# Optimization experiments

Hardware: AMD Instinct MI355X
Metric: run time of the kernel (lower is better)

The kernel has to match this reference:

```python
import jax, jax.numpy as jnp
import numpy as np

EMBED = 128
HEADS = 8
HEAD_DIM = EMBED // HEADS

def setup_inputs() -> dict:
    key = jax.random.key(0)
    ks = jax.random.split(key, 8)
    B, N = 2, 4096
    values = jax.random.normal(ks[0], (B, N, EMBED), dtype=jnp.float32)
    keys = jax.random.normal(ks[1], (B, N, EMBED), dtype=jnp.float32)
    query = jax.random.normal(ks[2], (B, N, EMBED), dtype=jnp.float32)
    s = 1.0 / np.sqrt(HEAD_DIM)
    Wv = jax.random.normal(ks[3], (HEAD_DIM, HEAD_DIM), dtype=jnp.float32) * s
    Wk = jax.random.normal(ks[4], (HEAD_DIM, HEAD_DIM), dtype=jnp.float32) * s
    Wq = jax.random.normal(ks[5], (HEAD_DIM, HEAD_DIM), dtype=jnp.float32) * s
    Wo = jax.random.normal(ks[6], (EMBED, EMBED), dtype=jnp.float32) * (1.0 / np.sqrt(EMBED))
    bo = jnp.zeros((EMBED,), dtype=jnp.float32)
    return {"values": values, "keys": keys, "query": query,
            "Wv": Wv, "Wk": Wk, "Wq": Wq, "Wo": Wo, "bo": bo}

def reference(values, keys, query, Wv, Wk, Wq, Wo, bo):
    B, N, _ = query.shape
    # split heads: [B,N,H,Dh]
    v = values.reshape(B, N, HEADS, HEAD_DIM)
    k = keys.reshape(B, N, HEADS, HEAD_DIM)
    q = query.reshape(B, N, HEADS, HEAD_DIM)
    # per-head linear (torch Linear: x @ W.T), same weight for all heads
    v = jnp.einsum('bnhd,ed->bnhe', v, Wv)
    k = jnp.einsum('bnhd,ed->bnhe', k, Wk)
    q = jnp.einsum('bnhd,ed->bnhe', q, Wq)
    # scores [B,H,N,N], note scale by sqrt(embed_size) as in original
    energy = jnp.einsum('bqhd,bkhd->bhqk', q, k) / jnp.sqrt(jnp.float32(EMBED))
    attn = jax.nn.softmax(energy, axis=-1)
    out = jnp.einsum('bhql,blhd->bqhd', attn, v).reshape(B, N, EMBED)
    return out @ Wo.T + bo
```

## Files before the change

### kernel.cpp

```cpp
#include <hip/hip_runtime.h>

#define BB 2
#define NN 4096
#define HH 8
#define DD 16
#define EE 128
#define LBLK 128
#define NSPL 4
#define NIV 4

typedef _Float16 f16;
typedef _Float16 f16x4 __attribute__((ext_vector_type(4)));
typedef _Float16 f16x2 __attribute__((ext_vector_type(2)));
typedef _Float16 f16x8 __attribute__((ext_vector_type(8)));
typedef __fp16 h16x2 __attribute__((ext_vector_type(2)));
typedef float f32x4 __attribute__((ext_vector_type(4)));

#define QSCALE 0.12751741f

__global__ __launch_bounds__(256) void proj_kernel(
    const float* __restrict__ vals, const float* __restrict__ keys,
    const float* __restrict__ query,
    const float* __restrict__ Wv, const float* __restrict__ Wk,
    const float* __restrict__ Wq, const float* __restrict__ Wo,
    f16* __restrict__ Qp, f16* __restrict__ Kp, f16* __restrict__ Vt,
    f16* __restrict__ Wo16)
{
    if (blockIdx.x >= 768) {
        const int i = (blockIdx.x - 768) * 256 + threadIdx.x;
        Wo16[i] = (f16)Wo[i];
        return;
    }
    __shared__ float W[256];
    const int p = blockIdx.x >> 8;
    const float* Wsrc = (p == 0) ? Wv : ((p == 1) ? Wk : Wq);
    W[threadIdx.x] = Wsrc[threadIdx.x];
    __syncthreads();

    const int idx = ((blockIdx.x & 255) << 8) | threadIdx.x;
    const int n = idx & 4095;
    const int h = (idx >> 12) & 7;
    const int b = idx >> 15;

    const float* xsrc = (p == 0) ? vals : ((p == 1) ? keys : query);
    const float4* xp = (const float4*)(xsrc + (size_t)(b * NN + n) * EE + h * DD);
    const float4 x0 = xp[0], x1 = xp[1], x2 = xp[2], x3 = xp[3];
    const float scale = (p == 2) ? QSCALE : 1.0f;

    alignas(16) f16 out[16];
    #pragma unroll
    for (int e = 0; e < 16; e++) {
        const float4* wr = (const float4*)(W + e * 16);
        const float4 w0 = wr[0], w1 = wr[1], w2 = wr[2], w3 = wr[3];
        float acc = x0.x * w0.x + x0.y * w0.y + x0.z * w0.z + x0.w * w0.w
                  + x1.x * w1.x + x1.y * w1.y + x1.z * w1.z + x1.w * w1.w
                  + x2.x * w2.x + x2.y * w2.y + x2.z * w2.z + x2.w * w2.w
                  + x3.x * w3.x + x3.y * w3.y + x3.z * w3.z + x3.w * w3.w;
        out[e] = (f16)(acc * scale);
    }

    if (p == 0) {
        f16* dst = Vt + (size_t)(b * HH + h) * DD * NN + n;
        #pragma unroll
        for (int e = 0; e < 16; e++) dst[(size_t)e * NN] = out[e];
    } else {
        f16* dst = ((p == 1) ? Kp : Qp) + (size_t)((b * HH + h) * NN + n) * DD;
        ((uint4*)dst)[0] = ((const uint4*)out)[0];
        ((uint4*)dst)[1] = ((const uint4*)out)[1];
    }
}

__global__ __launch_bounds__(512, 8) void attn_kernel(
    const f16* __restrict__ Qp, const f16* __restrict__ Kp,
    const f16* __restrict__ Vt, f16* __restrict__ Oacc,
    float* __restrict__ den)
{
    __shared__ alignas(16) f16 Kl[2][2][2048];
    __shared__ alignas(16) f16 Vl[2][2][2048];

    const int tid = threadIdx.x;
    const int lane = tid & 63;
    const int wave = tid >> 6;
    const int r = lane & 15;
    const int g = lane >> 4;

    const int bid = blockIdx.x;
    const int quarter = bid & 3;
    const int bh = (bid >> 2) & 15;
    const int qt = bid >> 6;
    const int q0 = qt * 256 + wave * 32;
    const int L0 = quarter * (NN / NSPL);

    const int ti = tid >> 8;
    const int u = tid & 255;
    const bool isK = u < 128;
    const f16* gbase;
    int w0, w1;
    if (isK) {
        const int spair = u >> 6;
        const int lp = u & 63;
        const int rr = lp & 15, gg = lp >> 4;
        const int lam = 8 * (rr >> 2) + (rr & 3);
        gbase = Kp + ((size_t)bh * NN + L0 + ti * LBLK + 64 * spair + lam) * DD + 4 * gg;
        w0 = (2 * spair) * 512 + lp * 8;
        w1 = (2 * spair + 1) * 512 + lp * 8;
    } else {
        const int v = u - 128;
        gbase = Vt + ((size_t)bh * DD + (v & 15)) * NN + L0 + ti * LBLK
                   + 32 * (v >> 6) + 8 * ((v >> 4) & 3);
        w0 = v * 8;
        w1 = 1024 + v * 8;
    }
    const size_t gstep = isK ? (size_t)(2 * LBLK) * DD : (size_t)(2 * LBLK);

    const f16x4 qf0 = *(const f16x4*)(Qp + ((size_t)bh * NN + q0 + r) * DD + 4 * g);
    const f16x4 qf1 = *(const f16x4*)(Qp + ((size_t)bh * NN + q0 + 16 + r) * DD + 4 * g);

    f16x8 sA, sB;
#define STAGE_LOAD() { \
    if (isK) { \
        const f16x4 a0 = *(const f16x4*)(gbase + 0); \
        const f16x4 a1 = *(const f16x4*)(gbase + 64); \
        const f16x4 a2 = *(const f16x4*)(gbase + 512); \
        const f16x4 a3 = *(const f16x4*)(gbase + 576); \
        sA = __builtin_shufflevector(a0, a1, 0,1,2,3,4,5,6,7); \
        sB = __builtin_shufflevector(a2, a3, 0,1,2,3,4,5,6,7); \
    } else { \
        sA = *(const f16x8*)(gbase + 0); \
        sB = *(const f16x8*)(gbase + 64); \
    } \
    gbase += gstep; }

#define STAGE_WRITE(HALF) { \
    f16* wp = isK ? &Kl[HALF][ti][0] : &Vl[HALF][ti][0]; \
    *(f16x8*)(wp + w0) = sA; \
    *(f16x8*)(wp + w1) = sB; }

    STAGE_LOAD();
    STAGE_WRITE(0);
    __syncthreads();

    f32x4 acc0 = {0.f,0.f,0.f,0.f}, acc1 = {0.f,0.f,0.f,0.f};
    f32x4 dacc0 = {0.f,0.f,0.f,0.f}, dacc1 = {0.f,0.f,0.f,0.f};
    const f32x4 zz = {0.f,0.f,0.f,0.f};
    const f16x8 ones8 = {(f16)1.f,(f16)1.f,(f16)1.f,(f16)1.f,
                         (f16)1.f,(f16)1.f,(f16)1.f,(f16)1.f};

#define QKPV(QF, ACC, DACC) { \
    const f32x4 st0 = __builtin_amdgcn_mfma_f32_16x16x16f16(kfA, (QF), zz, 0, 0, 0); \
    const f32x4 st1 = __builtin_amdgcn_mfma_f32_16x16x16f16(kfB, (QF), zz, 0, 0, 0); \
    const float e0 = __builtin_amdgcn_exp2f(st0[0]); \
    const float e1 = __builtin_amdgcn_exp2f(st0[1]); \
    const float e2 = __builtin_amdgcn_exp2f(st0[2]); \
    const float e3 = __builtin_amdgcn_exp2f(st0[3]); \
    const float f0 = __builtin_amdgcn_exp2f(st1[0]); \
    const float f1 = __builtin_amdgcn_exp2f(st1[1]); \
    const float f2 = __builtin_amdgcn_exp2f(st1[2]); \
    const float f3 = __builtin_amdgcn_exp2f(st1[3]); \
    const h16x2 h0 = __builtin_amdgcn_cvt_pkrtz(e0, e1); \
    const h16x2 h1 = __builtin_amdgcn_cvt_pkrtz(e2, e3); \
    const h16x2 h2 = __builtin_amdgcn_cvt_pkrtz(f0, f1); \
    const h16x2 h3 = __builtin_amdgcn_cvt_pkrtz(f2, f3); \
    const f16x4 pA = __builtin_shufflevector( \
        __builtin_bit_cast(f16x2, h0), __builtin_bit_cast(f16x2, h1), 0, 1, 2, 3); \
    const f16x4 pB = __builtin_shufflevector( \
        __builtin_bit_cast(f16x2, h2), __builtin_bit_cast(f16x2, h3), 0, 1, 2, 3); \
    const f16x8 pf8 = __builtin_shufflevector(pA, pB, 0, 1, 2, 3, 4, 5, 6, 7); \
    ACC  = __builtin_amdgcn_mfma_f32_16x16x32_f16(vf8, pf8, ACC, 0, 0, 0); \
    DACC = __builtin_amdgcn_mfma_f32_16x16x32_f16(ones8, pf8, DACC, 0, 0, 0); }

    int half = 0;
    for (int iv = 0; iv < NIV; ++iv) {
        if (iv < NIV - 1) STAGE_LOAD();

        __builtin_amdgcn_s_setprio(1);
        #pragma unroll
        for (int t2 = 0; t2 < 2; ++t2) {
            const f16* Kb = &Kl[half][t2][0];
            const f16* Vb = &Vl[half][t2][0];
            #pragma unroll
            for (int s = 0; s < 4; ++s) {
                const f16x8 kf8 = *(const f16x8*)(Kb + s * 512 + lane * 8);
                const f16x8 vf8 = *(const f16x8*)(Vb + s * 512 + lane * 8);
                const f16x4 kfA = __builtin_shufflevector(kf8, kf8, 0, 1, 2, 3);
                const f16x4 kfB = __builtin_shufflevector(kf8, kf8, 4, 5, 6, 7);
                QKPV(qf0, acc0, dacc0)
                QKPV(qf1, acc1, dacc1)
            }
        }
        __builtin_amdgcn_s_setprio(0);

        if (iv < NIV - 1) STAGE_WRITE(half ^ 1);
        __syncthreads();
        half ^= 1;
    }
#undef QKPV
#undef STAGE_WRITE
#undef STAGE_LOAD

    const int b = bh >> 3, h = bh & 7;
    f16* OaccQ = Oacc + (size_t)quarter * (BB * NN * EE);
    const f16x4 o0 = __builtin_shufflevector(
        __builtin_bit_cast(f16x2, __builtin_amdgcn_cvt_pkrtz(acc0[0], acc0[1])),
        __builtin_bit_cast(f16x2, __builtin_amdgcn_cvt_pkrtz(acc0[2], acc0[3])), 0, 1, 2, 3);
    const f16x4 o1 = __builtin_shufflevector(
        __builtin_bit_cast(f16x2, __builtin_amdgcn_cvt_pkrtz(acc1[0], acc1[1])),
        __builtin_bit_cast(f16x2, __builtin_amdgcn_cvt_pkrtz(acc1[2], acc1[3])), 0, 1, 2, 3);
    *(f16x4*)(OaccQ + ((size_t)(b * NN + q0 + r)) * EE + h * DD + 4 * g) = o0;
    *(f16x4*)(OaccQ + ((size_t)(b * NN + q0 + 16 + r)) * EE + h * DD + 4 * g) = o1;
    if (lane < 16) {
        den[(size_t)(quarter * 16 + bh) * NN + q0 + lane] = dacc0[0];
        den[(size_t)(quarter * 16 + bh) * NN + q0 + 16 + lane] = dacc1[0];
    }
}

static __device__ __forceinline__ f32x4 cvt4(f16x4 x) {
    return (f32x4){(float)x[0], (float)x[1], (float)x[2], (float)x[3]};
}

__global__ __launch_bounds__(256) void outproj_kernel(
    const f16* __restrict__ Oacc, const float* __restrict__ den,
    const f16* __restrict__ Wo16, const float* __restrict__ bo,
    float* __restrict__ out)
{
    const int lane = threadIdx.x & 63;
    const int wave = threadIdx.x >> 6;
    const int r = lane & 15;
    const int g = lane >> 4;
    const int n0 = (blockIdx.x * 2 + (wave >> 1)) * 16;
    const int eh = (wave & 1) * 4;

    const int n = n0 + r;
    const int b = n >> 12;
    const int nn = n & 4095;
    const f16* Oa0 = Oacc + (size_t)n * EE;
    const f16* Oa1 = Oa0 + (size_t)1 * (BB * NN * EE);
    const f16* Oa2 = Oa0 + (size_t)2 * (BB * NN * EE);
    const f16* Oa3 = Oa0 + (size_t)3 * (BB * NN * EE);

    f32x4 acc[4];
    #pragma unroll
    for (int e = 0; e < 4; e++) acc[e] = (f32x4){0.f, 0.f, 0.f, 0.f};

    #pragma unroll
    for (int k0 = 0; k0 < 8; k0++) {
        const size_t didx = (size_t)(b * 8 + k0) * NN + nn;
        const float inv = 1.0f / ((den[didx] + den[(size_t)16 * NN + didx])
                                + (den[(size_t)32 * NN + didx] + den[(size_t)48 * NN + didx]));
        const f32x4 xa = (cvt4(*(const f16x4*)(Oa0 + k0 * 16 + 4 * g))
                        + cvt4(*(const f16x4*)(Oa1 + k0 * 16 + 4 * g)))
                       + (cvt4(*(const f16x4*)(Oa2 + k0 * 16 + 4 * g))
                        + cvt4(*(const f16x4*)(Oa3 + k0 * 16 + 4 * g)));
        const float s0 = xa[0] * inv;
        const float s1 = xa[1] * inv;
        const float s2 = xa[2] * inv;
        const float s3 = xa[3] * inv;
        const f16x4 a = __builtin_shufflevector(
            __builtin_bit_cast(f16x2, __builtin_amdgcn_cvt_pkrtz(s0, s1)),
            __builtin_bit_cast(f16x2, __builtin_amdgcn_cvt_pkrtz(s2, s3)), 0, 1, 2, 3);
        #pragma unroll
        for (int e = 0; e < 4; e++) {
            const f16x4 bf = *(const f16x4*)(Wo16 + (size_t)((eh + e) * 16 + r) * EE + k0 * 16 + 4 * g);
            acc[e] = __builtin_amdgcn_mfma_f32_16x16x16f16(a, bf, acc[e], 0, 0, 0);
        }
    }

    #pragma unroll
    for (int e = 0; e < 4; e++) {
        const float bias = bo[(eh + e) * 16 + r];
        #pragma unroll
        for (int i = 0; i < 4; i++) {
            out[(size_t)(n0 + 4 * g + i) * EE + (eh + e) * 16 + r] = acc[e][i] + bias;
        }
    }
}

extern "C" void kernel_launch(void* const* d_in, const int* in_sizes, int n_in,
                              void* d_out, int out_size, void* d_ws, size_t ws_size,
                              hipStream_t stream)
{
    const float* vals  = (const float*)d_in[0];
    const float* keys  = (const float*)d_in[1];
    const float* query = (const float*)d_in[2];
    const float* Wv    = (const float*)d_in[3];
    const float* Wk    = (const float*)d_in[4];
    const float* Wq    = (const float*)d_in[5];
    const float* Wo    = (const float*)d_in[6];
    const float* bo    = (const float*)d_in[7];
    float* out = (float*)d_out;

    char* w = (char*)d_ws;
    f16*   Qp   = (f16*)(w);
    f16*   Kp   = (f16*)(w + (2u << 20));
    f16*   Vt   = (f16*)(w + (4u << 20));
    f16*   Wo16 = (f16*)(w + (6u << 20));
    float* den  = (float*)(w + (6u << 20) + 65536);
    f16*   Oacc = (f16*)(w + (8u << 20));

    hipLaunchKernelGGL(proj_kernel, dim3(832), dim3(256), 0, stream,
                       vals, keys, query, Wv, Wk, Wq, Wo, Qp, Kp, Vt, Wo16);
    hipLaunchKernelGGL(attn_kernel, dim3(1024), dim3(512), 0, stream,
                       Qp, Kp, Vt, Oacc, den);
    hipLaunchKernelGGL(outproj_kernel, dim3(256), dim3(256), 0, stream,
                       Oacc, den, Wo16, bo, out);
}
```

Baseline: 53.69 us.

## Give each attention wave 64 query rows and halve block size

The attention kernel now runs 256-thread blocks where each wave handles four 16-row query fragments instead of two. Each K/V tile loaded into shared memory is reused across more queries, and the staging ring shrinks to a single 128-key stage per buffer over 8 iterations. The output projection kernel is split so that each block covers 16 rows with 2 column tiles per wave, doubling the grid. This raises register pressure and lowers the number of waves per CU, and adds more sync points per key range.

```diff
diff --git a/kernel.cpp b/kernel.cpp
--- a/kernel.cpp
+++ b/kernel.cpp
@@ -7,7 +7,7 @@
 #define EE 128
 #define LBLK 128
 #define NSPL 4
-#define NIV 4
+#define NIV 8
 
 typedef _Float16 f16;
 typedef _Float16 f16x4 __attribute__((ext_vector_type(4)));
@@ -70,13 +70,13 @@
     }
 }
 
-__global__ __launch_bounds__(512, 8) void attn_kernel(
+__global__ __launch_bounds__(256, 4) void attn_kernel(
     const f16* __restrict__ Qp, const f16* __restrict__ Kp,
     const f16* __restrict__ Vt, f16* __restrict__ Oacc,
     float* __restrict__ den)
 {
-    __shared__ alignas(16) f16 Kl[2][2][2048];
-    __shared__ alignas(16) f16 Vl[2][2][2048];
+    __shared__ alignas(16) f16 Kl[2][2048];
+    __shared__ alignas(16) f16 Vl[2][2048];
 
     const int tid = threadIdx.x;
     const int lane = tid & 63;
@@ -88,33 +88,34 @@
     const int quarter = bid & 3;
     const int bh = (bid >> 2) & 15;
     const int qt = bid >> 6;
-    const int q0 = qt * 256 + wave * 32;
+    const int q0 = qt * 256 + wave * 64;
     const int L0 = quarter * (NN / NSPL);
 
-    const int ti = tid >> 8;
-    const int u = tid & 255;
-    const bool isK = u < 128;
+    const bool isK = tid < 128;
     const f16* gbase;
     int w0, w1;
     if (isK) {
-        const int spair = u >> 6;
-        const int lp = u & 63;
+        const int spair = tid >> 6;
+        const int lp = tid & 63;
         const int rr = lp & 15, gg = lp >> 4;
         const int lam = 8 * (rr >> 2) + (rr & 3);
-        gbase = Kp + ((size_t)bh * NN + L0 + ti * LBLK + 64 * spair + lam) * DD + 4 * gg;
+        gbase = Kp + ((size_t)bh * NN + L0 + 64 * spair + lam) * DD + 4 * gg;
         w0 = (2 * spair) * 512 + lp * 8;
         w1 = (2 * spair + 1) * 512 + lp * 8;
     } else {
-        const int v = u - 128;
-        gbase = Vt + ((size_t)bh * DD + (v & 15)) * NN + L0 + ti * LBLK
+        const int v = tid - 128;
+        gbase = Vt + ((size_t)bh * DD + (v & 15)) * NN + L0
                    + 32 * (v >> 6) + 8 * ((v >> 4) & 3);
         w0 = v * 8;
         w1 = 1024 + v * 8;
     }
-    const size_t gstep = isK ? (size_t)(2 * LBLK) * DD : (size_t)(2 * LBLK);
-
-    const f16x4 qf0 = *(const f16x4*)(Qp + ((size_t)bh * NN + q0 + r) * DD + 4 * g);
-    const f16x4 qf1 = *(const f16x4*)(Qp + ((size_t)bh * NN + q0 + 16 + r) * DD + 4 * g);
+    const size_t gstep = isK ? (size_t)LBLK * DD : (size_t)LBLK;
+
+    const f16* qbase = Qp + ((size_t)bh * NN + q0 + r) * DD + 4 * g;
+    const f16x4 qf0 = *(const f16x4*)(qbase);
+    const f16x4 qf1 = *(const f16x4*)(qbase + 16 * DD);
+    const f16x4 qf2 = *(const f16x4*)(qbase + 32 * DD);
+    const f16x4 qf3 = *(const f16x4*)(qbase + 48 * DD);
 
     f16x8 sA, sB;
 #define STAGE_LOAD() { \
@@ -132,7 +133,7 @@
     gbase += gstep; }
 
 #define STAGE_WRITE(HALF) { \
-    f16* wp = isK ? &Kl[HALF][ti][0] : &Vl[HALF][ti][0]; \
+    f16* wp = isK ? &Kl[HALF][0] : &Vl[HALF][0]; \
     *(f16x8*)(wp + w0) = sA; \
     *(f16x8*)(wp + w1) = sB; }
 
@@ -141,7 +142,9 @@
     __syncthreads();
 
     f32x4 acc0 = {0.f,0.f,0.f,0.f}, acc1 = {0.f,0.f,0.f,0.f};
+    f32x4 acc2 = {0.f,0.f,0.f,0.f}, acc3 = {0.f,0.f,0.f,0.f};
     f32x4 dacc0 = {0.f,0.f,0.f,0.f}, dacc1 = {0.f,0.f,0.f,0.f};
+    f32x4 dacc2 = {0.f,0.f,0.f,0.f}, dacc3 = {0.f,0.f,0.f,0.f};
     const f32x4 zz = {0.f,0.f,0.f,0.f};
     const f16x8 ones8 = {(f16)1.f,(f16)1.f,(f16)1.f,(f16)1.f,
                          (f16)1.f,(f16)1.f,(f16)1.f,(f16)1.f};
@@ -174,19 +177,18 @@
         if (iv < NIV - 1) STAGE_LOAD();
 
         __builtin_amdgcn_s_setprio(1);
+        const f16* Kb = &Kl[half][0];
+        const f16* Vb = &Vl[half][0];
         #pragma unroll
-        for (int t2 = 0; t2 < 2; ++t2) {
-            const f16* Kb = &Kl[half][t2][0];
-            const f16* Vb = &Vl[half][t2][0];
-            #pragma unroll
-            for (int s = 0; s < 4; ++s) {
-                const f16x8 kf8 = *(const f16x8*)(Kb + s * 512 + lane * 8);
-                const f16x8 vf8 = *(const f16x8*)(Vb + s * 512 + lane * 8);
-                const f16x4 kfA = __builtin_shufflevector(kf8, kf8, 0, 1, 2, 3);
-                const f16x4 kfB = __builtin_shufflevector(kf8, kf8, 4, 5, 6, 7);
-                QKPV(qf0, acc0, dacc0)
-                QKPV(qf1, acc1, dacc1)
-            }
+        for (int s = 0; s < 4; ++s) {
+            const f16x8 kf8 = *(const f16x8*)(Kb + s * 512 + lane * 8);
+            const f16x8 vf8 = *(const f16x8*)(Vb + s * 512 + lane * 8);
+            const f16x4 kfA = __builtin_shufflevector(kf8, kf8, 0, 1, 2, 3);
+            const f16x4 kfB = __builtin_shufflevector(kf8, kf8, 4, 5, 6, 7);
+            QKPV(qf0, acc0, dacc0)
+            QKPV(qf1, acc1, dacc1)
+            QKPV(qf2, acc2, dacc2)
+            QKPV(qf3, acc3, dacc3)
         }
         __builtin_amdgcn_s_setprio(0);
 
@@ -200,18 +202,19 @@
 
     const int b = bh >> 3, h = bh & 7;
     f16* OaccQ = Oacc + (size_t)quarter * (BB * NN * EE);
-    const f16x4 o0 = __builtin_shufflevector(
-        __builtin_bit_cast(f16x2, __builtin_amdgcn_cvt_pkrtz(acc0[0], acc0[1])),
-        __builtin_bit_cast(f16x2, __builtin_amdgcn_cvt_pkrtz(acc0[2], acc0[3])), 0, 1, 2, 3);
-    const f16x4 o1 = __builtin_shufflevector(
-        __builtin_bit_cast(f16x2, __builtin_amdgcn_cvt_pkrtz(acc1[0], acc1[1])),
-        __builtin_bit_cast(f16x2, __builtin_amdgcn_cvt_pkrtz(acc1[2], acc1[3])), 0, 1, 2, 3);
-    *(f16x4*)(OaccQ + ((size_t)(b * NN + q0 + r)) * EE + h * DD + 4 * g) = o0;
-    *(f16x4*)(OaccQ + ((size_t)(b * NN + q0 + 16 + r)) * EE + h * DD + 4 * g) = o1;
-    if (lane < 16) {
-        den[(size_t)(quarter * 16 + bh) * NN + q0 + lane] = dacc0[0];
-        den[(size_t)(quarter * 16 + bh) * NN + q0 + 16 + lane] = dacc1[0];
-    }
+#define STORE_FRAG(ACC, DACC, F) { \
+    const f16x4 o = __builtin_shufflevector( \
+        __builtin_bit_cast(f16x2, __builtin_amdgcn_cvt_pkrtz((ACC)[0], (ACC)[1])), \
+        __builtin_bit_cast(f16x2, __builtin_amdgcn_cvt_pkrtz((ACC)[2], (ACC)[3])), 0, 1, 2, 3); \
+    *(f16x4*)(OaccQ + ((size_t)(b * NN + q0 + 16 * (F) + r)) * EE + h * DD + 4 * g) = o; \
+    if (lane < 16) \
+        den[(size_t)(quarter * 16 + bh) * NN + q0 + 16 * (F) + lane] = (DACC)[0]; }
+
+    STORE_FRAG(acc0, dacc0, 0)
+    STORE_FRAG(acc1, dacc1, 1)
+    STORE_FRAG(acc2, dacc2, 2)
+    STORE_FRAG(acc3, dacc3, 3)
+#undef STORE_FRAG
 }
 
 static __device__ __forceinline__ f32x4 cvt4(f16x4 x) {
@@ -227,8 +230,8 @@
     const int wave = threadIdx.x >> 6;
     const int r = lane & 15;
     const int g = lane >> 4;
-    const int n0 = (blockIdx.x * 2 + (wave >> 1)) * 16;
-    const int eh = (wave & 1) * 4;
+    const int n0 = blockIdx.x * 16;
+    const int eh = wave * 2;
 
     const int n = n0 + r;
     const int b = n >> 12;
@@ -238,9 +241,9 @@
     const f16* Oa2 = Oa0 + (size_t)2 * (BB * NN * EE);
     const f16* Oa3 = Oa0 + (size_t)3 * (BB * NN * EE);
 
-    f32x4 acc[4];
-    #pragma unroll
-    for (int e = 0; e < 4; e++) acc[e] = (f32x4){0.f, 0.f, 0.f, 0.f};
+    f32x4 acc[2];
+    acc[0] = (f32x4){0.f, 0.f, 0.f, 0.f};
+    acc[1] = (f32x4){0.f, 0.f, 0.f, 0.f};
 
     #pragma unroll
     for (int k0 = 0; k0 < 8; k0++) {
@@ -259,14 +262,14 @@
             __builtin_bit_cast(f16x2, __builtin_amdgcn_cvt_pkrtz(s0, s1)),
             __builtin_bit_cast(f16x2, __builtin_amdgcn_cvt_pkrtz(s2, s3)), 0, 1, 2, 3);
         #pragma unroll
-        for (int e = 0; e < 4; e++) {
+        for (int e = 0; e < 2; e++) {
             const f16x4 bf = *(const f16x4*)(Wo16 + (size_t)((eh + e) * 16 + r) * EE + k0 * 16 + 4 * g);
             acc[e] = __builtin_amdgcn_mfma_f32_16x16x16f16(a, bf, acc[e], 0, 0, 0);
         }
     }
 
     #pragma unroll
-    for (int e = 0; e < 4; e++) {
+    for (int e = 0; e < 2; e++) {
         const float bias = bo[(eh + e) * 16 + r];
         #pragma unroll
         for (int i = 0; i < 4; i++) {
@@ -299,8 +302,8 @@
 
     hipLaunchKernelGGL(proj_kernel, dim3(832), dim3(256), 0, stream,
                        vals, keys, query, Wv, Wk, Wq, Wo, Qp, Kp, Vt, Wo16);
-    hipLaunchKernelGGL(attn_kernel, dim3(1024), dim3(512), 0, stream,
+    hipLaunchKernelGGL(attn_kernel, dim3(1024), dim3(256), 0, stream,
                        Qp, Kp, Vt, Oacc, den);
-    hipLaunchKernelGGL(outproj_kernel, dim3(256), dim3(256), 0, stream,
+    hipLaunchKernelGGL(outproj_kernel, dim3(512), dim3(256), 0, stream,
                        Oacc, den, Wo16, bo, out);
 }
```

Result: slower. 57.96 us (+8.0%).
